# Optimization experiments

Measured on AMD Instinct MI355X. Metric: run time of the kernel, lower is better.

## Reference

```python
import jax, jax.numpy as jnp
import numpy as np

EPS = 1e-5


def setup_inputs() -> dict:
    key = jax.random.key(0)
    k1, k2, k3 = jax.random.split(key, 3)
    B, D, T = 16, 256, 4096
    K = 2048
    x = jax.random.normal(k1, (B, D, T), dtype=jnp.float32)
    embedding_sum = jax.random.normal(k2, (K, D), dtype=jnp.float32)
    cluster_usage = jax.random.uniform(k3, (K,), dtype=jnp.float32)
    return {"x": x, "embedding_sum": embedding_sum, "cluster_usage": cluster_usage}


def reference(x, embedding_sum, cluster_usage):
    # embedding property: embedding_sum / clamp(cluster_usage, min=eps)
    emb = embedding_sum / jnp.clip(cluster_usage, EPS, None)[:, None]  # [K, D]
    B, D, T = x.shape
    x_flat = jnp.transpose(x, (0, 2, 1)).reshape(B * T, D)  # (b t) d
    # compute faithfully (clamped for numerical safety).
    x2 = jnp.sum(x_flat * x_flat, axis=-1, keepdims=True)      # [BT, 1]
    e2 = jnp.sum(emb * emb, axis=-1)                           # [K]
    d2 = x2 - 2.0 * (x_flat @ emb.T) + e2[None, :]             # [BT, K]
    distances = jnp.sqrt(jnp.clip(d2, 0.0, None))
    codes = jnp.argmin(distances, axis=-1).reshape(B, 1, T)    # int codes
    # decode: embedding gather, b t d -> b d t
    decoded = jnp.transpose(emb[codes[:, 0, :]], (0, 2, 1))    # [B, D, T]
    return codes, decoded
```

## Files before the change

### kernel.cpp

```cpp
#include <hip/hip_runtime.h>
#include <hip/hip_fp16.h>
#include <cmath>

#define EPS 1e-5f
#define TAU 0.15f
#define RP  8

#define Bn 16
#define Dn 256
#define Tn 4096
#define Kn 2048
#define NSLOT 16

typedef unsigned short ushort_t;
typedef __attribute__((ext_vector_type(8))) _Float16 f16x8;
typedef __attribute__((ext_vector_type(4))) float f32x4;

__device__ __forceinline__ unsigned short f2h(float v) {
    return __half_as_ushort(__float2half_rn(v));
}

__device__ __forceinline__ unsigned short f16_up(float v) {
    const __half h = __float2half_rn(v);
    const float back = __half2float(h);
    unsigned short u = __half_as_ushort(h);
    if (back < v) u = (u & 0x8000u) ? (u - 1) : (u + 1);
    return u;
}

#define GLOAD_LDS16(gp, lp) __builtin_amdgcn_global_load_lds( \
    (const __attribute__((address_space(1))) unsigned int*)(gp), \
    (__attribute__((address_space(3))) unsigned int*)(lp), 16, 0, 0)

__global__ __launch_bounds__(256) void prep_kernel(
    const float* __restrict__ es, const float* __restrict__ usage,
    float* __restrict__ emb, ushort_t* __restrict__ e16,
    float* __restrict__ bias, float4* __restrict__ embT4,
    int* __restrict__ counter)
{
    __shared__ float sh[256];
    __shared__ float wsum[4];
    const int k = blockIdx.x;
    const int d = threadIdx.x;
    const float inv = 1.0f / fmaxf(usage[k], EPS);
    const float v = es[(size_t)k * Dn + d] * inv;
    emb[(size_t)k * Dn + d] = v;
    e16[(size_t)k * Dn + d] = f2h(fminf(fmaxf(v, -65504.f), 65504.f));
    sh[d] = v;
    float sq = v * v;
    #pragma unroll
    for (int off = 32; off > 0; off >>= 1) sq += __shfl_down(sq, off, 64);
    const int lane = d & 63, wv = d >> 6;
    if (lane == 0) wsum[wv] = sq;
    __syncthreads();
    if (d < 64)
        embT4[(size_t)d * Kn + k] = make_float4(sh[4*d], sh[4*d+1], sh[4*d+2], sh[4*d+3]);
    if (d == 0) {
        bias[k] = 0.5f * (wsum[0] + wsum[1] + wsum[2] + wsum[3]);
        if (k == 0) *counter = 0;
    }
}

__global__ __launch_bounds__(256) void xsplit_kernel(
    const float* __restrict__ x, ushort_t* __restrict__ xh)
{
    __shared__ float tile[32 * 65];
    const int t0 = blockIdx.x * 64;
    const int d0 = blockIdx.y * 32;
    const int b  = blockIdx.z;
    const int tid = threadIdx.x;

    {
        const int dl = tid >> 3, tq = tid & 7;
        const float* src = x + ((size_t)(b * Dn + d0 + dl)) * Tn + t0 + tq * 8;
        const float4 a = *(const float4*)(src);
        const float4 c = *(const float4*)(src + 4);
        float* row = &tile[dl * 65 + tq * 8];
        row[0] = a.x; row[1] = a.y; row[2] = a.z; row[3] = a.w;
        row[4] = c.x; row[5] = c.y; row[6] = c.z; row[7] = c.w;
    }
    __syncthreads();
    {
        const int t_l = tid >> 2, dq = tid & 3;
        unsigned wh[4];
        #pragma unroll
        for (int i = 0; i < 4; ++i) {
            const float a = tile[(dq * 8 + 2 * i) * 65 + t_l];
            const float g = tile[(dq * 8 + 2 * i + 1) * 65 + t_l];
            wh[i] = (unsigned)f2h(a) | ((unsigned)f2h(g) << 16);
        }
        const size_t o = ((size_t)(b * Tn + t0 + t_l)) * Dn + d0 + dq * 8;
        *(uint4*)(xh + o) = make_uint4(wh[0], wh[1], wh[2], wh[3]);
    }
}

#define STAGE(q, d0)                                                          \
    {                                                                         \
        _Pragma("unroll")                                                     \
        for (int r = 0; r < 4; ++r) {                                         \
            const int cb = r * 512 + (wid << 6);                              \
            GLOAD_LDS16(xh + (bTt0 + srow[r]) * Dn + (d0) + scol[r],          \
                        &As[q][cb << 3]);                                     \
        }                                                                     \
        _Pragma("unroll")                                                     \
        for (int r = 0; r < 4; ++r) {                                         \
            const int cb = r * 512 + (wid << 6);                              \
            GLOAD_LDS16(e16 + ((size_t)(kbase + srow[r])) * Dn + (d0) + scol[r], \
                        &Bs[q][cb << 3]);                                     \
        }                                                                     \
    }

#define COMPUTE(q)                                                            \
    {                                                                         \
        _Pragma("unroll")                                                     \
        for (int sub = 0; sub < 2; ++sub) {                                   \
            const int slot8 = ((((sub << 2) | quad) ^ x7) << 3);              \
            f16x8 af[4]; f16x8 bf[8];                                         \
            _Pragma("unroll")                                                 \
            for (int i = 0; i < 4; ++i)                                       \
                af[i] = *(const f16x8*)(&As[q][aoffbase + (i << 10) + slot8]);\
            _Pragma("unroll")                                                 \
            for (int j = 0; j < 8; ++j)                                       \
                bf[j] = *(const f16x8*)(&Bs[q][boffbase + (j << 10) + slot8]);\
            __builtin_amdgcn_s_setprio(1);                                    \
            _Pragma("unroll")                                                 \
            for (int i = 0; i < 4; ++i)                                       \
                _Pragma("unroll")                                             \
                for (int j = 0; j < 8; ++j)                                   \
                    acc[i][j] = __builtin_amdgcn_mfma_f32_16x16x32_f16(       \
                        af[i], bf[j], acc[i][j], 0, 0, 0);                    \
            __builtin_amdgcn_s_setprio(0);                                    \
        }                                                                     \
    }

#define BARRIER_PIN()                                                         \
    __builtin_amdgcn_s_barrier();                                             \
    __builtin_amdgcn_sched_barrier(0)

__global__ __launch_bounds__(512, 2) void gemm_argmax(
    const ushort_t* __restrict__ xh, const ushort_t* __restrict__ e16,
    const float* __restrict__ bias, uint2* __restrict__ rec)
{
    __shared__ __align__(16) ushort_t As[2][256 * 64];
    __shared__ __align__(16) ushort_t Bs[2][256 * 64];

    const int bid   = blockIdx.x;
    const int xcd   = bid & 7;
    const int ks    = (bid >> 3) & 7;
    const int tilid = bid >> 6;
    const int gtile = tilid * 8 + xcd;
    const int b     = gtile >> 4;
    const int tt    = gtile & 15;
    const int t0    = tt << 8;
    const int kbase = ks << 8;

    const int tid  = threadIdx.x;
    const int lane = tid & 63;
    const int wid  = tid >> 6;
    const int l15  = lane & 15;
    const int quad = lane >> 4;
    const int wm   = wid >> 1;
    const int wn   = wid & 1;
    const int x7   = l15 & 7;

    const size_t bTt0 = (size_t)b * Tn + t0;

    int srow[4], scol[4];
    #pragma unroll
    for (int r = 0; r < 4; ++r) {
        const int c = r * 512 + tid;
        srow[r] = c >> 3;
        scol[r] = (((c & 7) ^ (srow[r] & 7)) << 3);
    }

    const int aoffbase = ((wm << 6) + l15) << 6;
    const int boffbase = ((wn << 7) + l15) << 6;

    f32x4 acc[4][8];
    #pragma unroll
    for (int i = 0; i < 4; ++i)
        #pragma unroll
        for (int j = 0; j < 8; ++j) acc[i][j] = (f32x4){0.f, 0.f, 0.f, 0.f};

    STAGE(0, 0);
    STAGE(1, 64);
    asm volatile("s_waitcnt vmcnt(8)" ::: "memory");
    BARRIER_PIN();
    COMPUTE(0);
    BARRIER_PIN();
    STAGE(0, 128);
    asm volatile("s_waitcnt vmcnt(8)" ::: "memory");
    BARRIER_PIN();
    COMPUTE(1);
    BARRIER_PIN();
    STAGE(1, 192);
    asm volatile("s_waitcnt vmcnt(8)" ::: "memory");
    BARRIER_PIN();
    COMPUTE(0);
    asm volatile("s_waitcnt vmcnt(0)" ::: "memory");
    BARRIER_PIN();
    COMPUTE(1);

    __builtin_amdgcn_sched_barrier(0);
    const int kw = kbase + (wn << 7);
    float bj[8];
    #pragma unroll
    for (int j = 0; j < 8; ++j) bj[j] = bias[kw + (j << 4) + l15];

    const int slot = (ks << 1) | wn;
    #pragma unroll
    for (int i = 0; i < 4; ++i) {
        float s1[4], s2[4]; int k1[4];
        #pragma unroll
        for (int r = 0; r < 4; ++r) { s1[r] = -INFINITY; s2[r] = -INFINITY; k1[r] = 0; }
        #pragma unroll
        for (int j = 0; j < 8; ++j) {
            const int kg = kw + (j << 4) + l15;
            #pragma unroll
            for (int r = 0; r < 4; ++r) {
                const float s = acc[i][j][r] - bj[j];
                if (s > s1[r]) { s2[r] = s1[r]; s1[r] = s; k1[r] = kg; }
                else if (s > s2[r]) s2[r] = s;
            }
        }
        #pragma unroll
        for (int m = 1; m <= 8; m <<= 1) {
            #pragma unroll
            for (int r = 0; r < 4; ++r) {
                const float os1 = __shfl_xor(s1[r], m);
                const float os2 = __shfl_xor(s2[r], m);
                const int   ok1 = __shfl_xor(k1[r], m);
                const bool take = (os1 > s1[r]) || (os1 == s1[r] && ok1 < k1[r]);
                const float ns2 = take ? fmaxf(s1[r], os2) : fmaxf(s2[r], os1);
                if (take) { s1[r] = os1; k1[r] = ok1; }
                s2[r] = ns2;
            }
        }
        if (l15 == 0) {
            #pragma unroll
            for (int r = 0; r < 4; ++r) {
                const int row = (wm << 6) + (i << 4) + (quad << 2) + r;
                uint2 e;
                e.x = __float_as_uint(s1[r]);
                e.y = ((unsigned)f16_up(s2[r]) << 16) | (unsigned)k1[r];
                rec[(size_t)slot * (Bn * Tn) + bTt0 + row] = e;
            }
        }
    }
}

__global__ __launch_bounds__(256) void merge_kernel(
    const uint2* __restrict__ rec, int* __restrict__ codes_i,
    float* __restrict__ codes_f, int* __restrict__ list, int* __restrict__ counter)
{
    const int p = blockIdx.x * 256 + threadIdx.x;
    uint2 e = rec[p];
    float g1 = __uint_as_float(e.x);
    float g2 = __half2float(__ushort_as_half((unsigned short)(e.y >> 16)));
    int kk = (int)(e.y & 0xffffu);
    #pragma unroll
    for (int s = 1; s < NSLOT; ++s) {
        e = rec[(size_t)s * (Bn * Tn) + p];
        const float s1 = __uint_as_float(e.x);
        if (s1 > g1) {
            const float s2u = __half2float(__ushort_as_half((unsigned short)(e.y >> 16)));
            g2 = fmaxf(fmaxf(g2, g1), s2u);
            g1 = s1;
            kk = (int)(e.y & 0xffffu);
        } else {
            g2 = fmaxf(g2, s1);
        }
    }
    codes_i[p] = kk;
    codes_f[p] = (float)kk;
    if (g1 - g2 < TAU) {
        const int idx = atomicAdd(counter, 1);
        list[idx] = p;
    }
}

__global__ __launch_bounds__(256) void rescue_kernel(
    const float* __restrict__ x, const float4* __restrict__ embT4,
    const float* __restrict__ bias, const int* __restrict__ list,
    const int* __restrict__ counter, int* __restrict__ codes_i,
    float* __restrict__ codes_f)
{
    __shared__ float xv[RP][256];
    __shared__ int plist[RP];
    __shared__ float rs[RP][4];
    __shared__ int   rk[RP][4];
    const int tid = threadIdx.x, lane = tid & 63, wid = tid >> 6;
    const int count = *counter;
    for (int base = blockIdx.x * RP; base < count; base += gridDim.x * RP) {
        const int npts = min(RP, count - base);
        __syncthreads();
        if (tid < npts) plist[tid] = list[base + tid];
        __syncthreads();
        for (int pi = 0; pi < npts; ++pi) {
            const int p = plist[pi];
            xv[pi][tid] = x[((size_t)((p >> 12) * Dn + tid)) * Tn + (p & 4095)];
        }
        for (int pi = npts; pi < RP; ++pi) xv[pi][tid] = 0.f;
        __syncthreads();

        float acc[8][RP];
        #pragma unroll
        for (int s = 0; s < 8; ++s)
            #pragma unroll
            for (int pi = 0; pi < RP; ++pi) acc[s][pi] = 0.f;

        for (int dc = 0; dc < 64; ++dc) {
            float4 ev[8];
            #pragma unroll
            for (int s = 0; s < 8; ++s)
                ev[s] = embT4[(size_t)dc * Kn + tid + (s << 8)];
            #pragma unroll
            for (int pi = 0; pi < RP; ++pi) {
                const float4 xw = *(const float4*)&xv[pi][dc << 2];
                #pragma unroll
                for (int s = 0; s < 8; ++s)
                    acc[s][pi] += ev[s].x * xw.x + ev[s].y * xw.y
                                + ev[s].z * xw.z + ev[s].w * xw.w;
            }
        }

        float bs[RP]; int bk[RP];
        #pragma unroll
        for (int pi = 0; pi < RP; ++pi) { bs[pi] = -INFINITY; bk[pi] = 0; }
        #pragma unroll
        for (int s = 0; s < 8; ++s) {
            const int kk = tid + (s << 8);
            const float bv = bias[kk];
            #pragma unroll
            for (int pi = 0; pi < RP; ++pi) {
                const float sc = acc[s][pi] - bv;
                if (sc > bs[pi]) { bs[pi] = sc; bk[pi] = kk; }
            }
        }
        #pragma unroll
        for (int off = 1; off < 64; off <<= 1) {
            #pragma unroll
            for (int pi = 0; pi < RP; ++pi) {
                const float os = __shfl_xor(bs[pi], off);
                const int   ok = __shfl_xor(bk[pi], off);
                if (os > bs[pi] || (os == bs[pi] && ok < bk[pi])) { bs[pi] = os; bk[pi] = ok; }
            }
        }
        if (lane == 0) {
            #pragma unroll
            for (int pi = 0; pi < RP; ++pi) { rs[pi][wid] = bs[pi]; rk[pi][wid] = bk[pi]; }
        }
        __syncthreads();
        if (tid < npts) {
            float fs = rs[tid][0]; int fk = rk[tid][0];
            #pragma unroll
            for (int w = 1; w < 4; ++w) {
                if (rs[tid][w] > fs || (rs[tid][w] == fs && rk[tid][w] < fk)) {
                    fs = rs[tid][w]; fk = rk[tid][w];
                }
            }
            const int p = plist[tid];
            codes_i[p] = fk;
            codes_f[p] = (float)fk;
        }
    }
}

__global__ __launch_bounds__(256) void decode_kernel(
    const float* __restrict__ emb, const int* __restrict__ codes,
    float* __restrict__ out)
{
    const int b = blockIdx.y;
    const int t = blockIdx.x * 256 + threadIdx.x;
    const int c = codes[(size_t)b * Tn + t];
    const float4* e4 = (const float4*)(emb + (size_t)c * Dn);
    float* ob = out + (size_t)b * Dn * Tn + t;
    #pragma unroll 4
    for (int d4 = 0; d4 < 64; ++d4) {
        const float4 v = e4[d4];
        ob[(size_t)(d4 * 4 + 0) * Tn] = v.x;
        ob[(size_t)(d4 * 4 + 1) * Tn] = v.y;
        ob[(size_t)(d4 * 4 + 2) * Tn] = v.z;
        ob[(size_t)(d4 * 4 + 3) * Tn] = v.w;
    }
}

extern "C" void kernel_launch(void* const* d_in, const int* in_sizes, int n_in,
                              void* d_out, int out_size, void* d_ws, size_t ws_size,
                              hipStream_t stream) {
    const float* x     = (const float*)d_in[0];
    const float* es    = (const float*)d_in[1];
    const float* usage = (const float*)d_in[2];

    char* ws = (char*)d_ws;
    float*    emb     = (float*)(ws + 0);
    float*    bias    = (float*)(ws + 2097152);
    ushort_t* e16     = (ushort_t*)(ws + 2105344);
    float4*   embT4   = (float4*)(ws + 3153920);
    int*      codes_i = (int*)(ws + 5251072);
    int*      list    = (int*)(ws + 5513216);
    int*      counter = (int*)(ws + 5775360);

    float* codes_f = (float*)d_out;
    float* decoded = (float*)d_out + (size_t)Bn * Tn;

    ushort_t* xh  = (ushort_t*)decoded;
    uint2*    rec = (uint2*)((char*)decoded + 33554432);

    prep_kernel<<<Kn, 256, 0, stream>>>(es, usage, emb, e16, bias, embT4, counter);

    dim3 gx(Tn / 64, Dn / 32, Bn);
    xsplit_kernel<<<gx, 256, 0, stream>>>(x, xh);

    gemm_argmax<<<2048, 512, 0, stream>>>(xh, e16, bias, rec);

    merge_kernel<<<(Bn * Tn) / 256, 256, 0, stream>>>(rec, codes_i, codes_f, list, counter);

    rescue_kernel<<<1024, 256, 0, stream>>>(x, embT4, bias, list, counter, codes_i, codes_f);

    dim3 g6(Tn / 256, Bn);
    decode_kernel<<<g6, 256, 0, stream>>>(emb, codes_i, decoded);
}
```

Before: 359.6 us.

## Fuse K-loop argmax into GEMM and drop the split-K merge kernel

Each GEMM block now walks all eight 256-code chunks itself instead of splitting codes across 8 blocks. The running top-1/top-2 argmax is updated in registers and interleaved with the next chunk's MFMAs, with the negated bias fed in as the accumulator seed. Two-way wave results are merged through LDS before writing codes and the rescue list directly. This removes the per-slot record writes and the separate merge kernel and launch. In exchange the grid shrinks to 256 blocks, giving one block per CU and less latency hiding, and register pressure rises.

```diff
diff --git a/kernel.cpp b/kernel.cpp
--- a/kernel.cpp
+++ b/kernel.cpp
@@ -10,7 +10,6 @@
 #define Dn 256
 #define Tn 4096
 #define Kn 2048
-#define NSLOT 16
 
 typedef unsigned short ushort_t;
 typedef __attribute__((ext_vector_type(8))) _Float16 f16x8;
@@ -18,14 +17,6 @@
 
 __device__ __forceinline__ unsigned short f2h(float v) {
     return __half_as_ushort(__float2half_rn(v));
-}
-
-__device__ __forceinline__ unsigned short f16_up(float v) {
-    const __half h = __float2half_rn(v);
-    const float back = __half2float(h);
-    unsigned short u = __half_as_ushort(h);
-    if (back < v) u = (u & 0x8000u) ? (u - 1) : (u + 1);
-    return u;
 }
 
 #define GLOAD_LDS16(gp, lp) __builtin_amdgcn_global_load_lds( \
@@ -94,43 +85,42 @@
     }
 }
 
-#define STAGE(q, d0)                                                          \
+#define STAGE(q, dd, kcc)                                                     \
     {                                                                         \
         _Pragma("unroll")                                                     \
         for (int r = 0; r < 4; ++r) {                                         \
             const int cb = r * 512 + (wid << 6);                              \
-            GLOAD_LDS16(xh + (bTt0 + srow[r]) * Dn + (d0) + scol[r],          \
+            GLOAD_LDS16(xh + (bTt0 + srow[r]) * Dn + (dd) + scol[r],          \
                         &As[q][cb << 3]);                                     \
         }                                                                     \
         _Pragma("unroll")                                                     \
         for (int r = 0; r < 4; ++r) {                                         \
             const int cb = r * 512 + (wid << 6);                              \
-            GLOAD_LDS16(e16 + ((size_t)(kbase + srow[r])) * Dn + (d0) + scol[r], \
+            GLOAD_LDS16(e16 + ((size_t)((kcc) * 256 + srow[r])) * Dn + (dd) + scol[r], \
                         &Bs[q][cb << 3]);                                     \
         }                                                                     \
     }
 
-#define COMPUTE(q)                                                            \
+#define COMPUTE_FULL(q)                                                       \
     {                                                                         \
+        __builtin_amdgcn_s_setprio(1);                                        \
         _Pragma("unroll")                                                     \
         for (int sub = 0; sub < 2; ++sub) {                                   \
             const int slot8 = ((((sub << 2) | quad) ^ x7) << 3);              \
-            f16x8 af[4]; f16x8 bf[8];                                         \
+            f16x8 af[4];                                                      \
             _Pragma("unroll")                                                 \
             for (int i = 0; i < 4; ++i)                                       \
                 af[i] = *(const f16x8*)(&As[q][aoffbase + (i << 10) + slot8]);\
             _Pragma("unroll")                                                 \
-            for (int j = 0; j < 8; ++j)                                       \
-                bf[j] = *(const f16x8*)(&Bs[q][boffbase + (j << 10) + slot8]);\
-            __builtin_amdgcn_s_setprio(1);                                    \
-            _Pragma("unroll")                                                 \
-            for (int i = 0; i < 4; ++i)                                       \
+            for (int j = 0; j < 8; ++j) {                                     \
+                const f16x8 bf = *(const f16x8*)(&Bs[q][boffbase + (j << 10) + slot8]); \
                 _Pragma("unroll")                                             \
-                for (int j = 0; j < 8; ++j)                                   \
+                for (int i = 0; i < 4; ++i)                                   \
                     acc[i][j] = __builtin_amdgcn_mfma_f32_16x16x32_f16(       \
-                        af[i], bf[j], acc[i][j], 0, 0, 0);                    \
-            __builtin_amdgcn_s_setprio(0);                                    \
+                        af[i], bf, acc[i][j], 0, 0, 0);                       \
+            }                                                                 \
         }                                                                     \
+        __builtin_amdgcn_s_setprio(0);                                        \
     }
 
 #define BARRIER_PIN()                                                         \
@@ -139,20 +129,21 @@
 
 __global__ __launch_bounds__(512, 2) void gemm_argmax(
     const ushort_t* __restrict__ xh, const ushort_t* __restrict__ e16,
-    const float* __restrict__ bias, uint2* __restrict__ rec)
+    const float* __restrict__ bias_g, int* __restrict__ codes_i,
+    float* __restrict__ codes_f, int* __restrict__ list,
+    int* __restrict__ counter)
 {
     __shared__ __align__(16) ushort_t As[2][256 * 64];
     __shared__ __align__(16) ushort_t Bs[2][256 * 64];
-
-    const int bid   = blockIdx.x;
-    const int xcd   = bid & 7;
-    const int ks    = (bid >> 3) & 7;
-    const int tilid = bid >> 6;
-    const int gtile = tilid * 8 + xcd;
-    const int b     = gtile >> 4;
-    const int tt    = gtile & 15;
-    const int t0    = tt << 8;
-    const int kbase = ks << 8;
+    __shared__ __align__(16) float    biasLds[2048];
+    __shared__ float rs1[2][256];
+    __shared__ float rs2[2][256];
+    __shared__ int   rk [2][256];
+
+    const int bid = blockIdx.x;
+    const int b   = bid >> 4;
+    const int tt  = bid & 15;
+    const int t0  = tt << 8;
 
     const int tid  = threadIdx.x;
     const int lane = tid & 63;
@@ -175,107 +166,164 @@
 
     const int aoffbase = ((wm << 6) + l15) << 6;
     const int boffbase = ((wn << 7) + l15) << 6;
-
+    const int kid0 = (wn << 7) + l15;
+
+    float S1[4][4], S2[4][4];
+    int   K1[4][4];
     f32x4 acc[4][8];
     #pragma unroll
     for (int i = 0; i < 4; ++i)
         #pragma unroll
-        for (int j = 0; j < 8; ++j) acc[i][j] = (f32x4){0.f, 0.f, 0.f, 0.f};
-
-    STAGE(0, 0);
-    STAGE(1, 64);
-    asm volatile("s_waitcnt vmcnt(8)" ::: "memory");
-    BARRIER_PIN();
-    COMPUTE(0);
-    BARRIER_PIN();
-    STAGE(0, 128);
-    asm volatile("s_waitcnt vmcnt(8)" ::: "memory");
-    BARRIER_PIN();
-    COMPUTE(1);
-    BARRIER_PIN();
-    STAGE(1, 192);
-    asm volatile("s_waitcnt vmcnt(8)" ::: "memory");
-    BARRIER_PIN();
-    COMPUTE(0);
-    asm volatile("s_waitcnt vmcnt(0)" ::: "memory");
-    BARRIER_PIN();
-    COMPUTE(1);
+        for (int r = 0; r < 4; ++r) { S1[i][r] = -INFINITY; S2[i][r] = -INFINITY; K1[i][r] = 0; }
+    #pragma unroll
+    for (int i = 0; i < 4; ++i)
+        #pragma unroll
+        for (int j = 0; j < 8; ++j)
+            acc[i][j] = (f32x4){-INFINITY, -INFINITY, -INFINITY, -INFINITY};
+
+    GLOAD_LDS16(bias_g + (tid << 2), biasLds + (wid << 8));
+    STAGE(0, 0, 0);
+    STAGE(1, 64, 0);
+
+    #pragma unroll 1
+    for (int kc = 0; kc < 8; ++kc) {
+        const int kid = kid0 + (kc << 8);
+
+        asm volatile("s_waitcnt vmcnt(8)" ::: "memory");
+        BARRIER_PIN();
+        {
+            float bj[8];
+            #pragma unroll
+            for (int j = 0; j < 8; ++j) bj[j] = biasLds[kid + (j << 4)];
+            __builtin_amdgcn_s_setprio(1);
+            #pragma unroll
+            for (int sub = 0; sub < 2; ++sub) {
+                const int slot8 = ((((sub << 2) | quad) ^ x7) << 3);
+                f16x8 af[4];
+                #pragma unroll
+                for (int i = 0; i < 4; ++i)
+                    af[i] = *(const f16x8*)(&As[0][aoffbase + (i << 10) + slot8]);
+                #pragma unroll
+                for (int j = 0; j < 8; ++j) {
+                    const f16x8 bf = *(const f16x8*)(&Bs[0][boffbase + (j << 10) + slot8]);
+                    if (sub == 0) {
+                        const int kpj = kid - 256 + (j << 4);
+                        const float nb = -bj[j];
+                        const f32x4 cin = {nb, nb, nb, nb};
+                        #pragma unroll
+                        for (int i = 0; i < 4; ++i) {
+                            #pragma unroll
+                            for (int r = 0; r < 4; ++r) {
+                                const float s  = acc[i][j][r];
+                                const float mn = fminf(s, S1[i][r]);
+                                S2[i][r] = fmaxf(S2[i][r], mn);
+                                const bool gt = s > S1[i][r];
+                                S1[i][r] = fmaxf(S1[i][r], s);
+                                K1[i][r] = gt ? kpj : K1[i][r];
+                            }
+                            acc[i][j] = __builtin_amdgcn_mfma_f32_16x16x32_f16(
+                                af[i], bf, cin, 0, 0, 0);
+                        }
+                    } else {
+                        #pragma unroll
+                        for (int i = 0; i < 4; ++i)
+                            acc[i][j] = __builtin_amdgcn_mfma_f32_16x16x32_f16(
+                                af[i], bf, acc[i][j], 0, 0, 0);
+                    }
+                }
+            }
+            __builtin_amdgcn_s_setprio(0);
+        }
+        BARRIER_PIN();
+        STAGE(0, 128, kc);
+
+        asm volatile("s_waitcnt vmcnt(8)" ::: "memory");
+        BARRIER_PIN();
+        COMPUTE_FULL(1);
+        BARRIER_PIN();
+        STAGE(1, 192, kc);
+
+        asm volatile("s_waitcnt vmcnt(8)" ::: "memory");
+        BARRIER_PIN();
+        COMPUTE_FULL(0);
+        BARRIER_PIN();
+        if (kc < 7) STAGE(0, 0, kc + 1);
+
+        if (kc < 7) { asm volatile("s_waitcnt vmcnt(8)" ::: "memory"); }
+        else        { asm volatile("s_waitcnt vmcnt(0)" ::: "memory"); }
+        BARRIER_PIN();
+        COMPUTE_FULL(1);
+        if (kc < 7) {
+            BARRIER_PIN();
+            STAGE(1, 64, kc + 1);
+        }
+    }
 
     __builtin_amdgcn_sched_barrier(0);
-    const int kw = kbase + (wn << 7);
-    float bj[8];
+
+    {
+        const int kfb = kid0 + 7 * 256;
+        #pragma unroll
+        for (int j = 0; j < 8; ++j) {
+            const int kfj = kfb + (j << 4);
+            #pragma unroll
+            for (int i = 0; i < 4; ++i)
+                #pragma unroll
+                for (int r = 0; r < 4; ++r) {
+                    const float s  = acc[i][j][r];
+                    const float mn = fminf(s, S1[i][r]);
+                    S2[i][r] = fmaxf(S2[i][r], mn);
+                    const bool gt = s > S1[i][r];
+                    S1[i][r] = fmaxf(S1[i][r], s);
+                    K1[i][r] = gt ? kfj : K1[i][r];
+                }
+        }
+    }
+
     #pragma unroll
-    for (int j = 0; j < 8; ++j) bj[j] = bias[kw + (j << 4) + l15];
-
-    const int slot = (ks << 1) | wn;
-    #pragma unroll
-    for (int i = 0; i < 4; ++i) {
-        float s1[4], s2[4]; int k1[4];
-        #pragma unroll
-        for (int r = 0; r < 4; ++r) { s1[r] = -INFINITY; s2[r] = -INFINITY; k1[r] = 0; }
-        #pragma unroll
-        for (int j = 0; j < 8; ++j) {
-            const int kg = kw + (j << 4) + l15;
+    for (int m = 1; m <= 8; m <<= 1) {
+        #pragma unroll
+        for (int i = 0; i < 4; ++i)
             #pragma unroll
             for (int r = 0; r < 4; ++r) {
-                const float s = acc[i][j][r] - bj[j];
-                if (s > s1[r]) { s2[r] = s1[r]; s1[r] = s; k1[r] = kg; }
-                else if (s > s2[r]) s2[r] = s;
-            }
-        }
-        #pragma unroll
-        for (int m = 1; m <= 8; m <<= 1) {
-            #pragma unroll
-            for (int r = 0; r < 4; ++r) {
-                const float os1 = __shfl_xor(s1[r], m);
-                const float os2 = __shfl_xor(s2[r], m);
-                const int   ok1 = __shfl_xor(k1[r], m);
-                const bool take = (os1 > s1[r]) || (os1 == s1[r] && ok1 < k1[r]);
-                const float ns2 = take ? fmaxf(s1[r], os2) : fmaxf(s2[r], os1);
-                if (take) { s1[r] = os1; k1[r] = ok1; }
-                s2[r] = ns2;
-            }
-        }
-        if (l15 == 0) {
+                const float os1 = __shfl_xor(S1[i][r], m);
+                const float os2 = __shfl_xor(S2[i][r], m);
+                const int   ok1 = __shfl_xor(K1[i][r], m);
+                const bool take = (os1 > S1[i][r]) || (os1 == S1[i][r] && ok1 < K1[i][r]);
+                const float ns2 = take ? fmaxf(S1[i][r], os2) : fmaxf(S2[i][r], os1);
+                if (take) { S1[i][r] = os1; K1[i][r] = ok1; }
+                S2[i][r] = ns2;
+            }
+    }
+
+    if (l15 == 0) {
+        #pragma unroll
+        for (int i = 0; i < 4; ++i)
             #pragma unroll
             for (int r = 0; r < 4; ++r) {
                 const int row = (wm << 6) + (i << 4) + (quad << 2) + r;
-                uint2 e;
-                e.x = __float_as_uint(s1[r]);
-                e.y = ((unsigned)f16_up(s2[r]) << 16) | (unsigned)k1[r];
-                rec[(size_t)slot * (Bn * Tn) + bTt0 + row] = e;
-            }
-        }
-    }
-}
-
-__global__ __launch_bounds__(256) void merge_kernel(
-    const uint2* __restrict__ rec, int* __restrict__ codes_i,
-    float* __restrict__ codes_f, int* __restrict__ list, int* __restrict__ counter)
-{
-    const int p = blockIdx.x * 256 + threadIdx.x;
-    uint2 e = rec[p];
-    float g1 = __uint_as_float(e.x);
-    float g2 = __half2float(__ushort_as_half((unsigned short)(e.y >> 16)));
-    int kk = (int)(e.y & 0xffffu);
-    #pragma unroll
-    for (int s = 1; s < NSLOT; ++s) {
-        e = rec[(size_t)s * (Bn * Tn) + p];
-        const float s1 = __uint_as_float(e.x);
-        if (s1 > g1) {
-            const float s2u = __half2float(__ushort_as_half((unsigned short)(e.y >> 16)));
-            g2 = fmaxf(fmaxf(g2, g1), s2u);
-            g1 = s1;
-            kk = (int)(e.y & 0xffffu);
-        } else {
-            g2 = fmaxf(g2, s1);
-        }
-    }
-    codes_i[p] = kk;
-    codes_f[p] = (float)kk;
-    if (g1 - g2 < TAU) {
-        const int idx = atomicAdd(counter, 1);
-        list[idx] = p;
+                rs1[wn][row] = S1[i][r];
+                rs2[wn][row] = S2[i][r];
+                rk [wn][row] = K1[i][r];
+            }
+    }
+    __syncthreads();
+
+    if (tid < 256) {
+        const int row = tid;
+        const float a1 = rs1[0][row], b1 = rs1[1][row];
+        const int   ka = rk[0][row],  kb = rk[1][row];
+        const bool tb = (b1 > a1) || (b1 == a1 && kb < ka);
+        const float w1 = tb ? b1 : a1;
+        const int   wk = tb ? kb : ka;
+        const float run = tb ? fmaxf(a1, rs2[1][row]) : fmaxf(b1, rs2[0][row]);
+        const size_t p = bTt0 + row;
+        codes_i[p] = wk;
+        codes_f[p] = (float)wk;
+        if (w1 - run < TAU) {
+            const int idx = atomicAdd(counter, 1);
+            list[idx] = (int)p;
+        }
     }
 }
 
@@ -405,16 +453,14 @@
     float* decoded = (float*)d_out + (size_t)Bn * Tn;
 
     ushort_t* xh  = (ushort_t*)decoded;
-    uint2*    rec = (uint2*)((char*)decoded + 33554432);
 
     prep_kernel<<<Kn, 256, 0, stream>>>(es, usage, emb, e16, bias, embT4, counter);
 
     dim3 gx(Tn / 64, Dn / 32, Bn);
     xsplit_kernel<<<gx, 256, 0, stream>>>(x, xh);
 
-    gemm_argmax<<<2048, 512, 0, stream>>>(xh, e16, bias, rec);
-
-    merge_kernel<<<(Bn * Tn) / 256, 256, 0, stream>>>(rec, codes_i, codes_f, list, counter);
+    gemm_argmax<<<256, 512, 0, stream>>>(xh, e16, bias, codes_i, codes_f,
+                                         list, counter);
 
     rescue_kernel<<<1024, 256, 0, stream>>>(x, embT4, bias, list, counter, codes_i, codes_f);
 
```

After: 567.2 us. 57.7% more time.
